# Kernel tuning notes

Hardware: AMD Instinct MI355X
Metric: run time of the kernel (lower is better)

The kernel has to match this reference:

```python
import jax, jax.numpy as jnp
import numpy as np
from jax import lax

HEADS = 8
DIM_HEAD = 64
INNER = HEADS * DIM_HEAD  # 512
LOG_SCALE_MAX = float(np.log(100.0))  # clamp for clamp_exp (SwinV2-style max temperature 1/0.01)
EPS_NORM = 1e-12  # F.normalize eps
EPS_LN = 1e-5


def setup_inputs() -> dict:
    key = jax.random.key(0)
    ks = jax.random.split(key, 6)
    b, c, h, w = 2, 256, 48, 48
    x = jax.random.normal(ks[0], (b, c, h, w), jnp.float32)
    w_in = jax.random.normal(ks[1], (3 * INNER, c), jnp.float32) * (c ** -0.5)
    b_in = jnp.zeros((3 * INNER,), jnp.float32)
    # learnable log-scale, init log(d_head ** -0.5), per head
    softmax_scale = jnp.full((HEADS, 1, 1), float(np.log(DIM_HEAD ** -0.5)), jnp.float32)
    w_dw = jax.random.normal(ks[2], (INNER, 1, 3, 3), jnp.float32) * (1.0 / 3.0)
    w_pw = jax.random.normal(ks[3], (2 * c, INNER), jnp.float32) * (INNER ** -0.5)
    gamma = jnp.full((2 * c,), 1e-3, jnp.float32)  # norm init_weight=0.001
    beta = jnp.zeros((2 * c,), jnp.float32)
    return {"x": x, "w_in": w_in, "b_in": b_in, "softmax_scale": softmax_scale,
            "w_dw": w_dw, "w_pw": w_pw, "gamma": gamma, "beta": beta}


def _l2norm(t):
    n = jnp.sqrt(jnp.sum(t * t, axis=-1, keepdims=True))
    return t / jnp.maximum(n, EPS_NORM)


def reference(x, w_in, b_in, softmax_scale, w_dw, w_pw, gamma, beta):
    b, c, h, w = x.shape
    s = h * w
    # proj_in: 1x1 conv then 'b (h c) x y -> b h x y c'
    y = jnp.einsum('bchw,oc->bohw', x, w_in) + b_in[None, :, None, None]
    y = y.reshape(b, HEADS, 3 * DIM_HEAD, h, w).transpose(0, 1, 3, 4, 2)  # b H x y (3*dh)
    y = y.reshape(b, HEADS, s, 3 * DIM_HEAD)
    q, k, v = jnp.split(y, 3, axis=-1)  # each [b, H, s, dh]
    # scaled cosine attention
    qn, kn = _l2norm(q), _l2norm(k)
    scale = jnp.exp(jnp.minimum(softmax_scale, LOG_SCALE_MAX))  # clamp_exp, [H,1,1]
    sim = jnp.einsum('bhid,bhjd->bhij', qn, kn) * scale[None]
    attn = jax.nn.softmax(sim, axis=-1)
    out = jnp.einsum('bhij,bhjd->bhid', attn, v)  # [b,H,s,dh]
    # unsplit heads -> 'b (h w) c' -> 'b c h w'
    update = out.transpose(0, 2, 1, 3).reshape(b, s, INNER)
    update = update.transpose(0, 2, 1).reshape(b, INNER, h, w)
    # proj_out: depthwise 3x3 (no bias) + pointwise 1x1 (no bias)
    dw = lax.conv_general_dilated(update, w_dw, (1, 1), 'SAME',
                                  feature_group_count=INNER,
                                  dimension_numbers=('NCHW', 'OIHW', 'NCHW'))
    pw = jnp.einsum('bchw,oc->bohw', dw, w_pw)  # [b, 2c, h, w]
    # channelwise layernorm with small init weight (norm_scales_and_shifts)
    mu = jnp.mean(pw, axis=1, keepdims=True)
    var = jnp.var(pw, axis=1, keepdims=True)
    normed = (pw - mu) * lax.rsqrt(var + EPS_LN)
    normed = normed * gamma[None, :, None, None] + beta[None, :, None, None]
    scales, shifts = jnp.split(normed, 2, axis=1)  # each [b, c, h, w]
    return shifts + x * scales
```

## Files before the change

### kernel.cpp

```cpp
#include <hip/hip_runtime.h>

#define B_ 2
#define C_ 256
#define S_ 2304
#define DH_ 64
#define O3_ 1536
#define INNER_ 512
#define LOGSMAX 4.605170185988092f
#define LOG2E 1.4426950408889634f

typedef __attribute__((ext_vector_type(8))) short short8;
typedef __attribute__((ext_vector_type(4))) float f32x4;
typedef __attribute__((ext_vector_type(16))) float f32x16;
typedef __attribute__((ext_vector_type(4))) unsigned short us4;
typedef __attribute__((ext_vector_type(2))) unsigned u32x2;
typedef __attribute__((ext_vector_type(4))) unsigned u32x4;
typedef __bf16 bf16x8 __attribute__((ext_vector_type(8)));

__device__ __forceinline__ unsigned short f2bf(float f) {
  unsigned u = __builtin_bit_cast(unsigned, f);
  u += 0x7FFFu + ((u >> 16) & 1u);
  return (unsigned short)(u >> 16);
}
__device__ __forceinline__ float bf2f(unsigned short h) {
  return __builtin_bit_cast(float, (unsigned)h << 16);
}
__device__ __forceinline__ bf16x8 as_bf(short8 v) {
  return __builtin_bit_cast(bf16x8, v);
}
__device__ __forceinline__ float fexp2(float x) {
#if __has_builtin(__builtin_amdgcn_exp2f)
  return __builtin_amdgcn_exp2f(x);
#else
  return __expf(x * 0.6931471805599453f);
#endif
}
__device__ __forceinline__ float frcp(float x) {
#if __has_builtin(__builtin_amdgcn_rcpf)
  return __builtin_amdgcn_rcpf(x);
#else
  return 1.f / x;
#endif
}
__device__ __forceinline__ unsigned pack_hi16(unsigned b, unsigned a) {
  return __builtin_amdgcn_perm(b, a, 0x07060302u);
}
__device__ __forceinline__ unsigned pk2(float a, float b) {
  unsigned ua = __builtin_bit_cast(unsigned, a) + 0x8000u;
  unsigned ub = __builtin_bit_cast(unsigned, b) + 0x8000u;
  return pack_hi16(ub, ua);
}

__global__ __launch_bounds__(256) void k_prep(const float* __restrict__ x,
                                              const float* __restrict__ w_in,
                                              const float* __restrict__ w_pw,
                                              unsigned short* __restrict__ xT,
                                              unsigned short* __restrict__ w_inb,
                                              unsigned short* __restrict__ w_pwb) {
  __shared__ float tile[64][65];
  int blk = blockIdx.x;
  int t = threadIdx.x;
  if (blk < 288) {
    int p0 = (blk % 36) * 64, c0 = ((blk / 36) % 4) * 64, b = blk / 144;
    const float* xb = x + (size_t)b * C_ * S_;
#pragma unroll
    for (int i = 0; i < 16; i++) {
      int c = i * 4 + (t >> 6);
      int p = t & 63;
      tile[c][p] = xb[(size_t)(c0 + c) * S_ + p0 + p];
    }
    __syncthreads();
    unsigned short* xTb = xT + (size_t)b * S_ * C_;
#pragma unroll
    for (int i = 0; i < 16; i++) {
      int p = i * 4 + (t >> 6);
      int c = t & 63;
      xTb[(size_t)(p0 + p) * C_ + c0 + c] = f2bf(tile[c][p]);
    }
  } else if (blk < 288 + 1536) {
    int i = (blk - 288) * 256 + t;
    w_inb[i] = f2bf(w_in[i]);
  } else {
    int i = (blk - 1824) * 256 + t;
    w_pwb[i] = f2bf(w_pw[i]);
  }
}

__global__ __launch_bounds__(256) void k_gemm_qkv(const unsigned short* __restrict__ A,
                                                  const unsigned short* __restrict__ BT,
                                                  const float* __restrict__ b_in,
                                                  const float* __restrict__ ss,
                                                  unsigned char* __restrict__ qn,
                                                  unsigned char* __restrict__ kn,
                                                  unsigned short* __restrict__ vT) {
  __shared__ __align__(16) unsigned short As[64][72];
  __shared__ __align__(16) unsigned short Bs[128][72];
  int t = threadIdx.x;
  int lane = t & 63, wv = t >> 6;
  int quad = lane >> 4, r15 = lane & 15;
  int by = blockIdx.y;
  int m0 = by * 64, n0 = blockIdx.x * 128;
  int b = blockIdx.z;
  const unsigned short* BTb = BT + (size_t)b * S_ * C_;

  f32x4 acc[4][2] = {};

  int srA = t >> 2, scA = (t & 3) * 16;
  int srB = t >> 1, scB = (t & 1) * 32;
  const unsigned short* ag = A + (size_t)(m0 + srA) * C_ + scA;
  const unsigned short* bg = BTb + (size_t)(n0 + srB) * C_ + scB;

  for (int k0 = 0; k0 < C_; k0 += 64) {
    short8 a0 = *(const short8*)(ag + k0);
    short8 a1 = *(const short8*)(ag + k0 + 8);
    short8 b0 = *(const short8*)(bg + k0);
    short8 b1 = *(const short8*)(bg + k0 + 8);
    short8 b2 = *(const short8*)(bg + k0 + 16);
    short8 b3 = *(const short8*)(bg + k0 + 24);
    __syncthreads();
    *(short8*)&As[srA][scA] = a0;
    *(short8*)&As[srA][scA + 8] = a1;
    *(short8*)&Bs[srB][scB] = b0;
    *(short8*)&Bs[srB][scB + 8] = b1;
    *(short8*)&Bs[srB][scB + 16] = b2;
    *(short8*)&Bs[srB][scB + 24] = b3;
    __syncthreads();
#pragma unroll
    for (int ks = 0; ks < 2; ks++) {
      short8 af[4], bfr[2];
#pragma unroll
      for (int i = 0; i < 4; i++) af[i] = *(const short8*)&As[i * 16 + r15][ks * 32 + quad * 8];
#pragma unroll
      for (int j = 0; j < 2; j++) bfr[j] = *(const short8*)&Bs[wv * 32 + j * 16 + r15][ks * 32 + quad * 8];
#pragma unroll
      for (int i = 0; i < 4; i++)
#pragma unroll
        for (int j = 0; j < 2; j++)
          acc[i][j] = __builtin_amdgcn_mfma_f32_16x16x32_bf16(as_bf(af[i]), as_bf(bfr[j]), acc[i][j], 0, 0, 0);
    }
  }

  int h = by / 3, seg = by - h * 3;
  int bh = b * 8 + h;
  f32x4 bi[4];
#pragma unroll
  for (int i = 0; i < 4; i++) bi[i] = *(const f32x4*)&b_in[m0 + i * 16 + quad * 4];
  float bv[4][2][4];
  float ssq0 = 0.f, ssq1 = 0.f;
#pragma unroll
  for (int i = 0; i < 4; i++)
#pragma unroll
    for (int rr = 0; rr < 4; rr++) {
      float v0 = acc[i][0][rr] + bi[i][rr];
      float v1 = acc[i][1][rr] + bi[i][rr];
      bv[i][0][rr] = v0;
      bv[i][1][rr] = v1;
      ssq0 += v0 * v0;
      ssq1 += v1 * v1;
    }
  if (seg < 2) {
    float sc = (seg == 0) ? __expf(fminf(ss[h], LOGSMAX)) * LOG2E : 1.f;
    ssq0 += __shfl_xor(ssq0, 16);
    ssq0 += __shfl_xor(ssq0, 32);
    ssq1 += __shfl_xor(ssq1, 16);
    ssq1 += __shfl_xor(ssq1, 32);
    float inv0 = sc / fmaxf(sqrtf(ssq0), 1e-12f);
    float inv1 = sc / fmaxf(sqrtf(ssq1), 1e-12f);
    unsigned char* dst = (seg == 0 ? qn : kn) + (size_t)bh * S_ * DH_;
#pragma unroll
    for (int i = 0; i < 4; i++)
#pragma unroll
      for (int j = 0; j < 2; j++) {
        float iv = j ? inv1 : inv0;
        int pk = __builtin_amdgcn_cvt_pk_fp8_f32(bv[i][j][0] * iv, bv[i][j][1] * iv, 0, false);
        pk = __builtin_amdgcn_cvt_pk_fp8_f32(bv[i][j][2] * iv, bv[i][j][3] * iv, pk, true);
        int p = n0 + wv * 32 + j * 16 + r15;
        *(int*)&dst[(size_t)p * DH_ + i * 16 + quad * 4] = pk;
      }
  } else {
    unsigned short* dst = vT + (size_t)bh * DH_ * S_;
#pragma unroll
    for (int i = 0; i < 4; i++)
#pragma unroll
      for (int j = 0; j < 2; j++) {
        int p = n0 + wv * 32 + j * 16 + r15;
#pragma unroll
        for (int rr = 0; rr < 4; rr++) {
          int d = i * 16 + quad * 4 + rr;
          dst[(size_t)d * S_ + p] = f2bf(bv[i][j][rr]);
        }
      }
  }
}

__global__ __launch_bounds__(128) void k_gemm2(const unsigned short* __restrict__ A,
                                               const unsigned short* __restrict__ BT,
                                               unsigned short* __restrict__ outp,
                                               int M, int N, int K) {
  __shared__ __align__(16) unsigned short As[64][72];
  __shared__ __align__(16) unsigned short Bs[64][72];
  int t = threadIdx.x;
  int lane = t & 63, wv = t >> 6;
  int quad = lane >> 4, r15 = lane & 15;
  int m0 = blockIdx.y * 64, n0 = blockIdx.x * 64;
  int b = blockIdx.z;
  const unsigned short* BTb = BT + (size_t)b * N * K;

  f32x4 acc[4][2] = {};

  int sr = t >> 1, sc = (t & 1) * 32;
  const unsigned short* ag = A + (size_t)(m0 + sr) * K + sc;
  const unsigned short* bg = BTb + (size_t)(n0 + sr) * K + sc;

  for (int k0 = 0; k0 < K; k0 += 64) {
    short8 a0 = *(const short8*)(ag + k0);
    short8 a1 = *(const short8*)(ag + k0 + 8);
    short8 a2 = *(const short8*)(ag + k0 + 16);
    short8 a3 = *(const short8*)(ag + k0 + 24);
    short8 b0 = *(const short8*)(bg + k0);
    short8 b1 = *(const short8*)(bg + k0 + 8);
    short8 b2 = *(const short8*)(bg + k0 + 16);
    short8 b3 = *(const short8*)(bg + k0 + 24);
    __syncthreads();
    *(short8*)&As[sr][sc] = a0;
    *(short8*)&As[sr][sc + 8] = a1;
    *(short8*)&As[sr][sc + 16] = a2;
    *(short8*)&As[sr][sc + 24] = a3;
    *(short8*)&Bs[sr][sc] = b0;
    *(short8*)&Bs[sr][sc + 8] = b1;
    *(short8*)&Bs[sr][sc + 16] = b2;
    *(short8*)&Bs[sr][sc + 24] = b3;
    __syncthreads();
#pragma unroll
    for (int ks = 0; ks < 2; ks++) {
      short8 af[4], bfr[2];
#pragma unroll
      for (int i = 0; i < 4; i++) af[i] = *(const short8*)&As[i * 16 + r15][ks * 32 + quad * 8];
#pragma unroll
      for (int j = 0; j < 2; j++) bfr[j] = *(const short8*)&Bs[wv * 32 + j * 16 + r15][ks * 32 + quad * 8];
#pragma unroll
      for (int i = 0; i < 4; i++)
#pragma unroll
        for (int j = 0; j < 2; j++)
          acc[i][j] = __builtin_amdgcn_mfma_f32_16x16x32_bf16(as_bf(af[i]), as_bf(bfr[j]), acc[i][j], 0, 0, 0);
    }
  }
  unsigned short* Cb = outp + (size_t)b * M * N;
#pragma unroll
  for (int i = 0; i < 4; i++)
#pragma unroll
    for (int j = 0; j < 2; j++)
#pragma unroll
      for (int rr = 0; rr < 4; rr++) {
        int row = m0 + i * 16 + quad * 4 + rr;
        int col = n0 + wv * 32 + j * 16 + r15;
        Cb[(size_t)row * N + col] = f2bf(acc[i][j][rr]);
      }
}

__global__ __launch_bounds__(256) void k_attn(const unsigned char* __restrict__ qn,
                                              const unsigned char* __restrict__ kn,
                                              const unsigned short* __restrict__ vT,
                                              const float* __restrict__ ss,
                                              unsigned short* __restrict__ attnp,
                                              float* __restrict__ lp) {
  __shared__ __align__(16) unsigned char Ks[64][72];
  __shared__ __align__(16) unsigned short Vs[64][72];
  int t = threadIdx.x;
  int w = t >> 6;
  int lane = t & 63;
  int l31 = lane & 31, hi = lane >> 5;
  int bh = blockIdx.x;
  int q0 = blockIdx.y * 128 + w * 32;
  int split = blockIdx.z;
  int ktbase = split * 9;
  const unsigned char* qb = qn + (size_t)bh * S_ * DH_;
  const unsigned char* kb = kn + (size_t)bh * S_ * DH_;
  const unsigned short* vb = vT + (size_t)bh * DH_ * S_;
  float shift2 = __expf(fminf(ss[bh & 7], LOGSMAX)) * LOG2E;

  const unsigned char* qrow = qb + (size_t)(q0 + l31) * DH_ + hi * 8;
  long qf[4];
#pragma unroll
  for (int ks = 0; ks < 4; ks++) qf[ks] = *(const long*)(qrow + ks * 16);

  const f32x16 z16 = {};
  f32x16 O0 = z16, O1 = z16;
  float l_part = 0.f;

  int srow = t >> 2;
  int scolK = (t & 3) * 16;
  int scolV = (t & 3) * 16;
  const unsigned char* kg = kb + ((size_t)(ktbase * 64) + srow) * DH_ + scolK;
  const unsigned short* vg = vb + (size_t)srow * S_ + ktbase * 64 + scolV;

  uint4 kr = *(const uint4*)kg;
  short8 vr0 = *(const short8*)vg;
  short8 vr1 = *(const short8*)(vg + 8);

  for (int i = 0; i < 9; i++) {
    __syncthreads();
    *(uint4*)&Ks[srow][scolK] = kr;
    *(short8*)&Vs[srow][scolV] = vr0;
    *(short8*)&Vs[srow][scolV + 8] = vr1;
    __syncthreads();
    if (i < 8) {
      kr = *(const uint4*)(kg + (size_t)(i + 1) * 64 * DH_);
      vr0 = *(const short8*)(vg + (i + 1) * 64);
      vr1 = *(const short8*)(vg + (i + 1) * 64 + 8);
    }
    f32x16 sc0, sc1;
    {
      long a0 = *(const long*)&Ks[l31][hi * 8];
      long a1 = *(const long*)&Ks[32 + l31][hi * 8];
      sc0 = __builtin_amdgcn_mfma_f32_32x32x16_fp8_fp8(a0, qf[0], z16, 0, 0, 0);
      sc1 = __builtin_amdgcn_mfma_f32_32x32x16_fp8_fp8(a1, qf[0], z16, 0, 0, 0);
    }
#pragma unroll
    for (int ks = 1; ks < 4; ks++) {
      long a0 = *(const long*)&Ks[l31][ks * 16 + hi * 8];
      long a1 = *(const long*)&Ks[32 + l31][ks * 16 + hi * 8];
      sc0 = __builtin_amdgcn_mfma_f32_32x32x16_fp8_fp8(a0, qf[ks], sc0, 0, 0, 0);
      sc1 = __builtin_amdgcn_mfma_f32_32x32x16_fp8_fp8(a1, qf[ks], sc1, 0, 0, 0);
    }
#pragma unroll
    for (int mt = 0; mt < 2; mt++) {
      const f32x16& s = mt ? sc1 : sc0;
      unsigned pk[8];
      float lsum = 0.f;
#pragma unroll
      for (int g2 = 0; g2 < 4; g2++) {
        float e0 = fexp2(s[g2 * 4 + 0] - shift2);
        float e1 = fexp2(s[g2 * 4 + 1] - shift2);
        float e2 = fexp2(s[g2 * 4 + 2] - shift2);
        float e3 = fexp2(s[g2 * 4 + 3] - shift2);
        lsum += (e0 + e1) + (e2 + e3);
        pk[2 * g2] = pk2(e0, e1);
        pk[2 * g2 + 1] = pk2(e2, e3);
      }
      l_part += lsum;
#pragma unroll
      for (int half = 0; half < 2; half++) {
        int gb = half * 4;
        unsigned ya = hi ? pk[gb + 0] : pk[gb + 2];
        unsigned yb = hi ? pk[gb + 1] : pk[gb + 3];
        unsigned ra = __shfl_xor(ya, 32);
        unsigned rb = __shfl_xor(yb, 32);
        u32x4 fd;
        fd[0] = hi ? ra : pk[gb + 0];
        fd[1] = hi ? rb : pk[gb + 1];
        fd[2] = hi ? pk[gb + 2] : ra;
        fd[3] = hi ? pk[gb + 3] : rb;
        short8 pb = __builtin_bit_cast(short8, fd);
        int ks = mt * 2 + half;
        short8 va0 = *(const short8*)&Vs[l31][ks * 16 + hi * 8];
        short8 va1 = *(const short8*)&Vs[32 + l31][ks * 16 + hi * 8];
        O0 = __builtin_amdgcn_mfma_f32_32x32x16_bf16(as_bf(va0), as_bf(pb), O0, 0, 0, 0);
        O1 = __builtin_amdgcn_mfma_f32_32x32x16_bf16(as_bf(va1), as_bf(pb), O1, 0, 0, 0);
      }
    }
  }
  float l = l_part + __shfl_xor(l_part, 32);
  if (hi == 0) lp[((size_t)(split * 16 + bh)) * S_ + q0 + l31] = l;
  unsigned short* orow = attnp + (((size_t)(split * 16 + bh)) * S_ + q0 + l31) * DH_;
#pragma unroll
  for (int mt = 0; mt < 2; mt++) {
    const f32x16& O = mt ? O1 : O0;
#pragma unroll
    for (int g = 0; g < 4; g++) {
      us4 o4 = {f2bf(O[g * 4 + 0]), f2bf(O[g * 4 + 1]), f2bf(O[g * 4 + 2]), f2bf(O[g * 4 + 3])};
      *(us4*)&orow[mt * 32 + g * 8 + hi * 4] = o4;
    }
  }
}

__global__ __launch_bounds__(256) void k_dwconv(const unsigned short* __restrict__ attnp,
                                                const float* __restrict__ lp,
                                                const float* __restrict__ w_dw,
                                                unsigned short* __restrict__ dwb) {
  int t = threadIdx.x;
  int d = t & 63;
  int pj = t >> 6;
  int p = blockIdx.y * 4 + pj;
  int bh = blockIdx.x;
  int b = bh >> 3, h = bh & 7;
  int yy = p / 48, xx = p % 48;
  const unsigned short* a0 = attnp + (size_t)bh * S_ * DH_ + d;
  const unsigned short* a1 = attnp + ((size_t)(16 + bh)) * S_ * DH_ + d;
  const unsigned short* a2 = attnp + ((size_t)(32 + bh)) * S_ * DH_ + d;
  const unsigned short* a3 = attnp + ((size_t)(48 + bh)) * S_ * DH_ + d;
  const float* l0 = lp + (size_t)bh * S_;
  const float* l1 = lp + (size_t)(16 + bh) * S_;
  const float* l2 = lp + (size_t)(32 + bh) * S_;
  const float* l3 = lp + (size_t)(48 + bh) * S_;
  int ch = h * 64 + d;
  float w[9];
#pragma unroll
  for (int i = 0; i < 9; i++) w[i] = w_dw[ch * 9 + i];
  float acc = 0.f;
#pragma unroll
  for (int dy = -1; dy <= 1; dy++) {
    int y2 = yy + dy;
    if (y2 < 0 || y2 >= 48) continue;
#pragma unroll
    for (int dx = -1; dx <= 1; dx++) {
      int x2 = xx + dx;
      if (x2 < 0 || x2 >= 48) continue;
      int p2 = y2 * 48 + x2;
      float rl = frcp(l0[p2] + l1[p2] + l2[p2] + l3[p2]);
      float v = (bf2f(a0[(size_t)p2 * DH_]) + bf2f(a1[(size_t)p2 * DH_]) +
                 bf2f(a2[(size_t)p2 * DH_]) + bf2f(a3[(size_t)p2 * DH_])) * rl;
      acc += v * w[(dy + 1) * 3 + dx + 1];
    }
  }
  dwb[((size_t)b * S_ + p) * INNER_ + ch] = f2bf(acc);
}

__global__ __launch_bounds__(256) void k_ln_final(const unsigned short* __restrict__ pw,
                                                  const float* __restrict__ gamma,
                                                  const float* __restrict__ beta,
                                                  const float* __restrict__ x,
                                                  float* __restrict__ out) {
  __shared__ float s_s0[32][8], s_s1[32][8], s_q0[32][8], s_q1[32][8];
  int t = threadIdx.x;
  int pl = t & 7, g = t >> 3;
  int b = blockIdx.y;
  int p = blockIdx.x * 16 + pl * 2;
  const unsigned short* pwb = pw + (size_t)b * INNER_ * S_ + p;
  float s0 = 0.f, s1 = 0.f, q0 = 0.f, q1 = 0.f;
#pragma unroll
  for (int j = 0; j < 16; j++) {
    unsigned u = *(const unsigned*)&pwb[(size_t)(g * 16 + j) * S_];
    float vx = bf2f((unsigned short)(u & 0xffffu));
    float vy = bf2f((unsigned short)(u >> 16));
    s0 += vx; s1 += vy;
    q0 += vx * vx; q1 += vy * vy;
  }
  s_s0[g][pl] = s0; s_s1[g][pl] = s1;
  s_q0[g][pl] = q0; s_q1[g][pl] = q1;
  __syncthreads();
  float t0 = 0.f, t1 = 0.f, u0 = 0.f, u1 = 0.f;
#pragma unroll
  for (int i = 0; i < 32; i++) {
    t0 += s_s0[i][pl]; t1 += s_s1[i][pl];
    u0 += s_q0[i][pl]; u1 += s_q1[i][pl];
  }
  float mu0 = t0 * (1.f / 512.f), mu1 = t1 * (1.f / 512.f);
  float rs0 = rsqrtf(u0 * (1.f / 512.f) - mu0 * mu0 + 1e-5f);
  float rs1 = rsqrtf(u1 * (1.f / 512.f) - mu1 * mu1 + 1e-5f);
  const float* xb = x + (size_t)b * C_ * S_ + p;
  float* ob = out + (size_t)b * C_ * S_ + p;
#pragma unroll
  for (int j = 0; j < 8; j++) {
    int cc = g * 8 + j;
    float ga = gamma[cc], be = beta[cc];
    float gs = gamma[cc + 256], bs = beta[cc + 256];
    unsigned pu = *(const unsigned*)&pwb[(size_t)cc * S_];
    unsigned su = *(const unsigned*)&pwb[(size_t)(cc + 256) * S_];
    float2 xv = *(const float2*)&xb[(size_t)cc * S_];
    float pv0 = bf2f((unsigned short)(pu & 0xffffu));
    float pv1 = bf2f((unsigned short)(pu >> 16));
    float sv0 = bf2f((unsigned short)(su & 0xffffu));
    float sv1 = bf2f((unsigned short)(su >> 16));
    float sc0 = (pv0 - mu0) * rs0 * ga + be;
    float sc1 = (pv1 - mu1) * rs1 * ga + be;
    float sh0 = (sv0 - mu0) * rs0 * gs + bs;
    float sh1 = (sv1 - mu1) * rs1 * gs + bs;
    float2 o;
    o.x = sh0 + xv.x * sc0;
    o.y = sh1 + xv.y * sc1;
    *(float2*)&ob[(size_t)cc * S_] = o;
  }
}

extern "C" void kernel_launch(void* const* d_in, const int* in_sizes, int n_in,
                              void* d_out, int out_size, void* d_ws, size_t ws_size,
                              hipStream_t stream) {
  const float* x = (const float*)d_in[0];
  const float* w_in = (const float*)d_in[1];
  const float* b_in = (const float*)d_in[2];
  const float* ss = (const float*)d_in[3];
  const float* w_dw = (const float*)d_in[4];
  const float* w_pw = (const float*)d_in[5];
  const float* gamma = (const float*)d_in[6];
  const float* beta = (const float*)d_in[7];
  float* out = (float*)d_out;
  char* ws = (char*)d_ws;

  unsigned short* xT = (unsigned short*)(ws + 0);
  unsigned short* w_inb = (unsigned short*)(ws + 2359296);
  unsigned short* w_pwb = (unsigned short*)(ws + 3145728);
  unsigned char* qn = (unsigned char*)(ws + 3670016);
  unsigned char* kn = (unsigned char*)(ws + 6029312);
  unsigned short* vT = (unsigned short*)(ws + 8388608);
  unsigned short* dwb = (unsigned short*)(ws + 13107200);
  float* lp = (float*)(ws + 17825792);
  unsigned short* attnp = (unsigned short*)(ws + 18415616);
  unsigned short* pw = (unsigned short*)(ws + 37289984);

  k_prep<<<2848, 256, 0, stream>>>(x, w_in, w_pw, xT, w_inb, w_pwb);
  k_gemm_qkv<<<dim3(18, 24, 2), 256, 0, stream>>>(w_inb, xT, b_in, ss, qn, kn, vT);
  k_attn<<<dim3(16, 18, 4), 256, 0, stream>>>(qn, kn, vT, ss, attnp, lp);
  k_dwconv<<<dim3(16, 576), 256, 0, stream>>>(attnp, lp, w_dw, dwb);
  k_gemm2<<<dim3(36, 8, 2), 128, 0, stream>>>(w_pwb, dwb, pw, INNER_, S_, INNER_);
  k_ln_final<<<dim3(144, 2), 256, 0, stream>>>(pw, gamma, beta, x, out);
}
```

Measured before the change: 160.9 us.

## Double query rows per attention wave and stage V transpose through LDS

The attention kernel now has each wave process two 32-row query tiles against every K/V tile loaded into shared memory. This halves the K/V staging traffic and the syncs per query, and the grid shrinks to match. In the QKV GEMM epilogue, the scattered 2-byte transposed stores of V are replaced by writing into reused shared memory first, then emitting coalesced 16-byte rows. The costs are higher register pressure and half as many attention blocks (576), which may hurt occupancy and latency hiding.

After: 177.9 us. 1.11x slower.

```diff
diff --git a/kernel.cpp b/kernel.cpp
--- a/kernel.cpp
+++ b/kernel.cpp
@@ -13,7 +13,6 @@
 typedef __attribute__((ext_vector_type(4))) float f32x4;
 typedef __attribute__((ext_vector_type(16))) float f32x16;
 typedef __attribute__((ext_vector_type(4))) unsigned short us4;
-typedef __attribute__((ext_vector_type(2))) unsigned u32x2;
 typedef __attribute__((ext_vector_type(4))) unsigned u32x4;
 typedef __bf16 bf16x8 __attribute__((ext_vector_type(8)));
 
@@ -93,8 +92,9 @@
                                                   unsigned char* __restrict__ qn,
                                                   unsigned char* __restrict__ kn,
                                                   unsigned short* __restrict__ vT) {
-  __shared__ __align__(16) unsigned short As[64][72];
-  __shared__ __align__(16) unsigned short Bs[128][72];
+  __shared__ __align__(16) unsigned short smem[64 * 72 + 128 * 72];
+  unsigned short (*As)[72] = (unsigned short(*)[72])smem;
+  unsigned short (*Bs)[72] = (unsigned short(*)[72])(smem + 64 * 72);
   int t = threadIdx.x;
   int lane = t & 63, wv = t >> 6;
   int quad = lane >> 4, r15 = lane & 15;
@@ -178,18 +178,27 @@
         *(int*)&dst[(size_t)p * DH_ + i * 16 + quad * 4] = pk;
       }
   } else {
-    unsigned short* dst = vT + (size_t)bh * DH_ * S_;
+    __syncthreads();
+    unsigned short* vt = smem;
 #pragma unroll
     for (int i = 0; i < 4; i++)
 #pragma unroll
       for (int j = 0; j < 2; j++) {
-        int p = n0 + wv * 32 + j * 16 + r15;
+        int pcol = wv * 32 + j * 16 + r15;
 #pragma unroll
         for (int rr = 0; rr < 4; rr++) {
           int d = i * 16 + quad * 4 + rr;
-          dst[(size_t)d * S_ + p] = f2bf(bv[i][j][rr]);
+          vt[d * 132 + pcol] = f2bf(bv[i][j][rr]);
         }
       }
+    __syncthreads();
+    unsigned short* dst = vT + (size_t)bh * DH_ * S_;
+    int dr = t >> 2, pc = (t & 3) * 32;
+#pragma unroll
+    for (int s2 = 0; s2 < 4; s2++) {
+      short8 v8 = *(const short8*)&vt[dr * 132 + pc + s2 * 8];
+      *(short8*)&dst[(size_t)dr * S_ + n0 + pc + s2 * 8] = v8;
+    }
   }
 }
 
@@ -271,7 +280,8 @@
   int lane = t & 63;
   int l31 = lane & 31, hi = lane >> 5;
   int bh = blockIdx.x;
-  int q0 = blockIdx.y * 128 + w * 32;
+  int q0A = blockIdx.y * 256 + w * 32;
+  int q0B = q0A + 128;
   int split = blockIdx.z;
   int ktbase = split * 9;
   const unsigned char* qb = qn + (size_t)bh * S_ * DH_;
@@ -279,14 +289,18 @@
   const unsigned short* vb = vT + (size_t)bh * DH_ * S_;
   float shift2 = __expf(fminf(ss[bh & 7], LOGSMAX)) * LOG2E;
 
-  const unsigned char* qrow = qb + (size_t)(q0 + l31) * DH_ + hi * 8;
-  long qf[4];
-#pragma unroll
-  for (int ks = 0; ks < 4; ks++) qf[ks] = *(const long*)(qrow + ks * 16);
+  const unsigned char* qrowA = qb + (size_t)(q0A + l31) * DH_ + hi * 8;
+  const unsigned char* qrowB = qb + (size_t)(q0B + l31) * DH_ + hi * 8;
+  long qfA[4], qfB[4];
+#pragma unroll
+  for (int ks = 0; ks < 4; ks++) {
+    qfA[ks] = *(const long*)(qrowA + ks * 16);
+    qfB[ks] = *(const long*)(qrowB + ks * 16);
+  }
 
   const f32x16 z16 = {};
-  f32x16 O0 = z16, O1 = z16;
-  float l_part = 0.f;
+  f32x16 OA0 = z16, OA1 = z16, OB0 = z16, OB1 = z16;
+  float lA = 0.f, lB = 0.f;
 
   int srow = t >> 2;
   int scolK = (t & 3) * 16;
@@ -309,67 +323,93 @@
       vr0 = *(const short8*)(vg + (i + 1) * 64);
       vr1 = *(const short8*)(vg + (i + 1) * 64 + 8);
     }
-    f32x16 sc0, sc1;
-    {
-      long a0 = *(const long*)&Ks[l31][hi * 8];
-      long a1 = *(const long*)&Ks[32 + l31][hi * 8];
-      sc0 = __builtin_amdgcn_mfma_f32_32x32x16_fp8_fp8(a0, qf[0], z16, 0, 0, 0);
-      sc1 = __builtin_amdgcn_mfma_f32_32x32x16_fp8_fp8(a1, qf[0], z16, 0, 0, 0);
-    }
-#pragma unroll
-    for (int ks = 1; ks < 4; ks++) {
-      long a0 = *(const long*)&Ks[l31][ks * 16 + hi * 8];
-      long a1 = *(const long*)&Ks[32 + l31][ks * 16 + hi * 8];
-      sc0 = __builtin_amdgcn_mfma_f32_32x32x16_fp8_fp8(a0, qf[ks], sc0, 0, 0, 0);
-      sc1 = __builtin_amdgcn_mfma_f32_32x32x16_fp8_fp8(a1, qf[ks], sc1, 0, 0, 0);
-    }
 #pragma unroll
     for (int mt = 0; mt < 2; mt++) {
-      const f32x16& s = mt ? sc1 : sc0;
-      unsigned pk[8];
-      float lsum = 0.f;
+      f32x16 sA, sB;
+      {
+        long a = *(const long*)&Ks[mt * 32 + l31][hi * 8];
+        sA = __builtin_amdgcn_mfma_f32_32x32x16_fp8_fp8(a, qfA[0], z16, 0, 0, 0);
+        sB = __builtin_amdgcn_mfma_f32_32x32x16_fp8_fp8(a, qfB[0], z16, 0, 0, 0);
+      }
+#pragma unroll
+      for (int ks = 1; ks < 4; ks++) {
+        long a = *(const long*)&Ks[mt * 32 + l31][ks * 16 + hi * 8];
+        sA = __builtin_amdgcn_mfma_f32_32x32x16_fp8_fp8(a, qfA[ks], sA, 0, 0, 0);
+        sB = __builtin_amdgcn_mfma_f32_32x32x16_fp8_fp8(a, qfB[ks], sB, 0, 0, 0);
+      }
+      unsigned pkA[8], pkB[8];
+      float lsA = 0.f, lsB = 0.f;
 #pragma unroll
       for (int g2 = 0; g2 < 4; g2++) {
-        float e0 = fexp2(s[g2 * 4 + 0] - shift2);
-        float e1 = fexp2(s[g2 * 4 + 1] - shift2);
-        float e2 = fexp2(s[g2 * 4 + 2] - shift2);
-        float e3 = fexp2(s[g2 * 4 + 3] - shift2);
-        lsum += (e0 + e1) + (e2 + e3);
-        pk[2 * g2] = pk2(e0, e1);
-        pk[2 * g2 + 1] = pk2(e2, e3);
-      }
-      l_part += lsum;
+        float a0 = fexp2(sA[g2 * 4 + 0] - shift2);
+        float a1 = fexp2(sA[g2 * 4 + 1] - shift2);
+        float a2 = fexp2(sA[g2 * 4 + 2] - shift2);
+        float a3 = fexp2(sA[g2 * 4 + 3] - shift2);
+        lsA += (a0 + a1) + (a2 + a3);
+        pkA[2 * g2] = pk2(a0, a1);
+        pkA[2 * g2 + 1] = pk2(a2, a3);
+        float b0 = fexp2(sB[g2 * 4 + 0] - shift2);
+        float b1 = fexp2(sB[g2 * 4 + 1] - shift2);
+        float b2 = fexp2(sB[g2 * 4 + 2] - shift2);
+        float b3 = fexp2(sB[g2 * 4 + 3] - shift2);
+        lsB += (b0 + b1) + (b2 + b3);
+        pkB[2 * g2] = pk2(b0, b1);
+        pkB[2 * g2 + 1] = pk2(b2, b3);
+      }
+      lA += lsA;
+      lB += lsB;
 #pragma unroll
       for (int half = 0; half < 2; half++) {
         int gb = half * 4;
-        unsigned ya = hi ? pk[gb + 0] : pk[gb + 2];
-        unsigned yb = hi ? pk[gb + 1] : pk[gb + 3];
-        unsigned ra = __shfl_xor(ya, 32);
-        unsigned rb = __shfl_xor(yb, 32);
-        u32x4 fd;
-        fd[0] = hi ? ra : pk[gb + 0];
-        fd[1] = hi ? rb : pk[gb + 1];
-        fd[2] = hi ? pk[gb + 2] : ra;
-        fd[3] = hi ? pk[gb + 3] : rb;
-        short8 pb = __builtin_bit_cast(short8, fd);
+        unsigned yaA = hi ? pkA[gb + 0] : pkA[gb + 2];
+        unsigned ybA = hi ? pkA[gb + 1] : pkA[gb + 3];
+        unsigned raA = __shfl_xor(yaA, 32);
+        unsigned rbA = __shfl_xor(ybA, 32);
+        u32x4 fdA;
+        fdA[0] = hi ? raA : pkA[gb + 0];
+        fdA[1] = hi ? rbA : pkA[gb + 1];
+        fdA[2] = hi ? pkA[gb + 2] : raA;
+        fdA[3] = hi ? pkA[gb + 3] : rbA;
+        short8 pbA = __builtin_bit_cast(short8, fdA);
+        unsigned yaB = hi ? pkB[gb + 0] : pkB[gb + 2];
+        unsigned ybB = hi ? pkB[gb + 1] : pkB[gb + 3];
+        unsigned raB = __shfl_xor(yaB, 32);
+        unsigned rbB = __shfl_xor(ybB, 32);
+        u32x4 fdB;
+        fdB[0] = hi ? raB : pkB[gb + 0];
+        fdB[1] = hi ? rbB : pkB[gb + 1];
+        fdB[2] = hi ? pkB[gb + 2] : raB;
+        fdB[3] = hi ? pkB[gb + 3] : rbB;
+        short8 pbB = __builtin_bit_cast(short8, fdB);
         int ks = mt * 2 + half;
         short8 va0 = *(const short8*)&Vs[l31][ks * 16 + hi * 8];
         short8 va1 = *(const short8*)&Vs[32 + l31][ks * 16 + hi * 8];
-        O0 = __builtin_amdgcn_mfma_f32_32x32x16_bf16(as_bf(va0), as_bf(pb), O0, 0, 0, 0);
-        O1 = __builtin_amdgcn_mfma_f32_32x32x16_bf16(as_bf(va1), as_bf(pb), O1, 0, 0, 0);
-      }
-    }
-  }
-  float l = l_part + __shfl_xor(l_part, 32);
-  if (hi == 0) lp[((size_t)(split * 16 + bh)) * S_ + q0 + l31] = l;
-  unsigned short* orow = attnp + (((size_t)(split * 16 + bh)) * S_ + q0 + l31) * DH_;
+        OA0 = __builtin_amdgcn_mfma_f32_32x32x16_bf16(as_bf(va0), as_bf(pbA), OA0, 0, 0, 0);
+        OA1 = __builtin_amdgcn_mfma_f32_32x32x16_bf16(as_bf(va1), as_bf(pbA), OA1, 0, 0, 0);
+        OB0 = __builtin_amdgcn_mfma_f32_32x32x16_bf16(as_bf(va0), as_bf(pbB), OB0, 0, 0, 0);
+        OB1 = __builtin_amdgcn_mfma_f32_32x32x16_bf16(as_bf(va1), as_bf(pbB), OB1, 0, 0, 0);
+      }
+    }
+  }
+  float lAt = lA + __shfl_xor(lA, 32);
+  float lBt = lB + __shfl_xor(lB, 32);
+  size_t lbase = ((size_t)(split * 16 + bh)) * S_;
+  if (hi == 0) {
+    lp[lbase + q0A + l31] = lAt;
+    lp[lbase + q0B + l31] = lBt;
+  }
+  unsigned short* orowA = attnp + (lbase + q0A + l31) * DH_;
+  unsigned short* orowB = attnp + (lbase + q0B + l31) * DH_;
 #pragma unroll
   for (int mt = 0; mt < 2; mt++) {
-    const f32x16& O = mt ? O1 : O0;
+    const f32x16& OA = mt ? OA1 : OA0;
+    const f32x16& OB = mt ? OB1 : OB0;
 #pragma unroll
     for (int g = 0; g < 4; g++) {
-      us4 o4 = {f2bf(O[g * 4 + 0]), f2bf(O[g * 4 + 1]), f2bf(O[g * 4 + 2]), f2bf(O[g * 4 + 3])};
-      *(us4*)&orow[mt * 32 + g * 8 + hi * 4] = o4;
+      us4 oa = {f2bf(OA[g * 4 + 0]), f2bf(OA[g * 4 + 1]), f2bf(OA[g * 4 + 2]), f2bf(OA[g * 4 + 3])};
+      *(us4*)&orowA[mt * 32 + g * 8 + hi * 4] = oa;
+      us4 ob = {f2bf(OB[g * 4 + 0]), f2bf(OB[g * 4 + 1]), f2bf(OB[g * 4 + 2]), f2bf(OB[g * 4 + 3])};
+      *(us4*)&orowB[mt * 32 + g * 8 + hi * 4] = ob;
     }
   }
 }
@@ -500,7 +540,7 @@
 
   k_prep<<<2848, 256, 0, stream>>>(x, w_in, w_pw, xT, w_inb, w_pwb);
   k_gemm_qkv<<<dim3(18, 24, 2), 256, 0, stream>>>(w_inb, xT, b_in, ss, qn, kn, vT);
-  k_attn<<<dim3(16, 18, 4), 256, 0, stream>>>(qn, kn, vT, ss, attnp, lp);
+  k_attn<<<dim3(16, 9, 4), 256, 0, stream>>>(qn, kn, vT, ss, attnp, lp);
   k_dwconv<<<dim3(16, 576), 256, 0, stream>>>(attnp, lp, w_dw, dwb);
   k_gemm2<<<dim3(36, 8, 2), 128, 0, stream>>>(w_pwb, dwb, pw, INNER_, S_, INNER_);
   k_ln_final<<<dim3(144, 2), 256, 0, stream>>>(pw, gamma, beta, x, out);
```
